# Kernel optimization log

Measured on AMD Instinct MI355X. Metric: run time of the kernel, lower is better.

## Reference

```python
import jax, jax.numpy as jnp
import numpy as np

N, C, H, K = 100000, 64, 8, 16
D = C // H  # head_dim = 8


def setup_inputs() -> dict:
    key = jax.random.key(0)
    ks = jax.random.split(key, 7)
    s = 1.0 / np.sqrt(C)
    return {
        "feats": jax.random.normal(ks[0], (N, C), jnp.float32),
        "knn_idx": jax.random.randint(ks[1], (N, K), 0, N, jnp.int32),
        "Wq": jax.random.normal(ks[2], (C, C), jnp.float32) * s,
        "Wk": jax.random.normal(ks[3], (C, C), jnp.float32) * s,
        "Wv": jax.random.normal(ks[4], (C, C), jnp.float32) * s,
        "Wo": jax.random.normal(ks[5], (C, C), jnp.float32) * s,
        "bo": jnp.zeros((C,), jnp.float32),
    }


def reference(feats, knn_idx, Wq, Wk, Wv, Wo, bo):
    # Projections (torch Linear y = x @ W^T expressed with pre-transposed W)
    q = (feats @ Wq).reshape(N, H, D)          # [N,H,D]
    k_feat = (feats @ Wk).reshape(N, H, D)     # [N,H,D]
    v = (feats @ Wv).reshape(N, H, D)          # [N,H,D]

    # Gather k-NN neighbors: [N,K,H,D]
    k_nb = k_feat[knn_idx]
    v_nb = v[knn_idx]

    # Scores: dot(q, k_neighbor) per head, scaled
    scores = jnp.einsum("nhd,nkhd->nkh", q, k_nb) / np.sqrt(D).astype(np.float32)
    attn = jax.nn.softmax(scores, axis=1)      # softmax over K neighbors

    out = jnp.einsum("nkh,nkhd->nhd", attn, v_nb).reshape(N, C)
    return out @ Wo + bo
```

## Files before the change

### kernel.cpp

```cpp
#include <hip/hip_runtime.h>
#include <hip/hip_fp16.h>
#include <math.h>

#define NPTS 100000
#define CDIM 64
#define KNN  16

typedef unsigned int uint;
typedef _Float16 f16x8 __attribute__((ext_vector_type(8)));
typedef float    f32x4 __attribute__((ext_vector_type(4)));

template <int CTRL>
__device__ __forceinline__ float dpp_add(float x) {
    int yi = __builtin_amdgcn_mov_dpp(__float_as_int(x), CTRL, 0xF, 0xF, true);
    return x + __int_as_float(yi);
}


__global__ __launch_bounds__(256) void pack_w(
    const float* __restrict__ Wq, const float* __restrict__ Wk,
    const float* __restrict__ Wv, const float* __restrict__ Wo,
    __half* __restrict__ frag)
{
    const float* Ws[4] = {Wq, Wk, Wv, Wo};
    f16x8* fp = (f16x8*)frag;
    const int e = blockIdx.x * 256 + threadIdx.x;
    const int lane = e & 63;
    const int ks   = (e >> 6) & 1;
    const int ct   = (e >> 7) & 3;
    const int mat  = e >> 9;
    const int m = lane & 15, quad = lane >> 4;
    const float* W = Ws[mat];
    f16x8 b;
    #pragma unroll
    for (int j = 0; j < 8; ++j)
        b[j] = (_Float16)W[(size_t)(ks * 32 + quad * 8 + j) * 64 + ct * 16 + m];
    fp[e] = b;
}

__device__ __forceinline__ f16x8 load_bfeat(const float* fp, int ks, int quad) {
    const float4 x0 = *(const float4*)(fp + ks * 32 + quad * 8);
    const float4 x1 = *(const float4*)(fp + ks * 32 + quad * 8 + 4);
    f16x8 a;
    a[0] = (_Float16)x0.x; a[1] = (_Float16)x0.y;
    a[2] = (_Float16)x0.z; a[3] = (_Float16)x0.w;
    a[4] = (_Float16)x1.x; a[5] = (_Float16)x1.y;
    a[6] = (_Float16)x1.z; a[7] = (_Float16)x1.w;
    return a;
}

__global__ __launch_bounds__(256) void proj_qkv(
    const float* __restrict__ feats, const __half* __restrict__ frag,
    __half* __restrict__ q, uint* __restrict__ kv)
{
    const int wid = blockIdx.x * 4 + (threadIdx.x >> 6);
    if (wid >= NPTS / 16) return;
    const int lane = threadIdx.x & 63;
    const int m = lane & 15, quad = lane >> 4;

    const f16x8* fp = (const f16x8*)frag;
    f16x8 Wf[3][4][2];
    #pragma unroll
    for (int mat = 0; mat < 3; ++mat)
        #pragma unroll
        for (int ct = 0; ct < 4; ++ct)
            #pragma unroll
            for (int ks = 0; ks < 2; ++ks)
                Wf[mat][ct][ks] = fp[((mat * 4 + ct) * 2 + ks) * 64 + lane];

    const int r0 = wid * 16;
    const float* ap = feats + (size_t)(r0 + m) * 64;
    const f16x8 Bf0 = load_bfeat(ap, 0, quad);
    const f16x8 Bf1 = load_bfeat(ap, 1, quad);

    const size_t pt = (size_t)(r0 + m);

    #pragma unroll
    for (int ct = 0; ct < 4; ++ct) {
        f32x4 aq = {0.f, 0.f, 0.f, 0.f};
        f32x4 ak = {0.f, 0.f, 0.f, 0.f};
        f32x4 av = {0.f, 0.f, 0.f, 0.f};
        aq = __builtin_amdgcn_mfma_f32_16x16x32_f16(Wf[0][ct][0], Bf0, aq, 0, 0, 0);
        aq = __builtin_amdgcn_mfma_f32_16x16x32_f16(Wf[0][ct][1], Bf1, aq, 0, 0, 0);
        ak = __builtin_amdgcn_mfma_f32_16x16x32_f16(Wf[1][ct][0], Bf0, ak, 0, 0, 0);
        ak = __builtin_amdgcn_mfma_f32_16x16x32_f16(Wf[1][ct][1], Bf1, ak, 0, 0, 0);
        av = __builtin_amdgcn_mfma_f32_16x16x32_f16(Wf[2][ct][0], Bf0, av, 0, 0, 0);
        av = __builtin_amdgcn_mfma_f32_16x16x32_f16(Wf[2][ct][1], Bf1, av, 0, 0, 0);

        const int ch = ct * 16 + quad * 4;
        uint2 qp;
        qp.x = (uint)__half_as_ushort(__float2half(aq[0]))
             | ((uint)__half_as_ushort(__float2half(aq[1])) << 16);
        qp.y = (uint)__half_as_ushort(__float2half(aq[2]))
             | ((uint)__half_as_ushort(__float2half(aq[3])) << 16);
        *(uint2*)(q + pt * 64 + ch) = qp;
        uint4 kp;
        kp.x = (uint)__half_as_ushort(__float2half(ak[0]))
             | ((uint)__half_as_ushort(__float2half(av[0])) << 16);
        kp.y = (uint)__half_as_ushort(__float2half(ak[1]))
             | ((uint)__half_as_ushort(__float2half(av[1])) << 16);
        kp.z = (uint)__half_as_ushort(__float2half(ak[2]))
             | ((uint)__half_as_ushort(__float2half(av[2])) << 16);
        kp.w = (uint)__half_as_ushort(__float2half(ak[3]))
             | ((uint)__half_as_ushort(__float2half(av[3])) << 16);
        *(uint4*)(kv + pt * 64 + ch) = kp;
    }
}

__global__ __launch_bounds__(256) void attn_out(
    const __half* __restrict__ q, const uint* __restrict__ kv,
    const int* __restrict__ knn, const __half* __restrict__ frag,
    const float* __restrict__ bo, float* __restrict__ out)
{
    __shared__ float sO[16][68];
    const int t = threadIdx.x;
    const int lane = t & 63;
    const int w = t >> 6;
    const int m = lane & 15, quad = lane >> 4;

    const f16x8* fpb = (const f16x8*)frag;
    const f16x8 Wf0 = fpb[((3 * 4 + w) * 2 + 0) * 64 + lane];
    const f16x8 Wf1 = fpb[((3 * 4 + w) * 2 + 1) * 64 + lane];

    const int n0 = blockIdx.x * 16;
    const float SC = 0.3535533905932738f * 1.4426950408889634f;

    #pragma unroll 1
    for (int p = 0; p < 4; ++p) {
        const int n = n0 + w * 4 + p;
        const int ns = __builtin_amdgcn_readfirstlane(n);

        const float qv = __half2float(q[(size_t)n * 64 + lane]);

        const int* kr = knn + (size_t)ns * KNN;
        int idx[KNN];
        #pragma unroll
        for (int i = 0; i < KNN; ++i) idx[i] = kr[i];

        uint u[KNN];
        #pragma unroll
        for (int i = 0; i < KNN; ++i) u[i] = kv[(size_t)idx[i] * 64 + lane];

        float sc[KNN], vr[KNN];
        #pragma unroll
        for (int i = 0; i < KNN; ++i) {
            const float2 kvf = __half22float2(*(const __half2*)&u[i]);
            vr[i] = kvf.y;
            float pr = qv * kvf.x;
            pr = dpp_add<0xB1>(pr);
            pr = dpp_add<0x4E>(pr);
            pr = dpp_add<0x141>(pr);
            sc[i] = __builtin_amdgcn_exp2f(pr * SC);
        }

        float s = 0.f;
        #pragma unroll
        for (int i = 0; i < KNN; ++i) s += sc[i];
        const float inv = 1.f / s;

        float acc = 0.f;
        #pragma unroll
        for (int i = 0; i < KNN; ++i) acc += sc[i] * vr[i];

        sO[w * 4 + p][lane] = acc * inv;
    }
    __syncthreads();

    f16x8 Bf0, Bf1;
    {
        const float* ap = &sO[m][0];
        const float4 x0 = *(const float4*)(ap + quad * 8);
        const float4 x1 = *(const float4*)(ap + quad * 8 + 4);
        Bf0[0] = (_Float16)x0.x; Bf0[1] = (_Float16)x0.y;
        Bf0[2] = (_Float16)x0.z; Bf0[3] = (_Float16)x0.w;
        Bf0[4] = (_Float16)x1.x; Bf0[5] = (_Float16)x1.y;
        Bf0[6] = (_Float16)x1.z; Bf0[7] = (_Float16)x1.w;
        const float4 y0 = *(const float4*)(ap + 32 + quad * 8);
        const float4 y1 = *(const float4*)(ap + 32 + quad * 8 + 4);
        Bf1[0] = (_Float16)y0.x; Bf1[1] = (_Float16)y0.y;
        Bf1[2] = (_Float16)y0.z; Bf1[3] = (_Float16)y0.w;
        Bf1[4] = (_Float16)y1.x; Bf1[5] = (_Float16)y1.y;
        Bf1[6] = (_Float16)y1.z; Bf1[7] = (_Float16)y1.w;
    }

    f32x4 ac = {0.f, 0.f, 0.f, 0.f};
    ac = __builtin_amdgcn_mfma_f32_16x16x32_f16(Wf0, Bf0, ac, 0, 0, 0);
    ac = __builtin_amdgcn_mfma_f32_16x16x32_f16(Wf1, Bf1, ac, 0, 0, 0);

    const int ch = w * 16 + quad * 4;
    const float4 bias = *(const float4*)(bo + ch);
    float4 o;
    o.x = ac[0] + bias.x; o.y = ac[1] + bias.y;
    o.z = ac[2] + bias.z; o.w = ac[3] + bias.w;
    *(float4*)(out + (size_t)(n0 + m) * 64 + ch) = o;
}

extern "C" void kernel_launch(void* const* d_in, const int* in_sizes, int n_in,
                              void* d_out, int out_size, void* d_ws, size_t ws_size,
                              hipStream_t stream) {
    const float* feats = (const float*)d_in[0];
    const int*   knn   = (const int*)d_in[1];
    const float* Wq    = (const float*)d_in[2];
    const float* Wk    = (const float*)d_in[3];
    const float* Wv    = (const float*)d_in[4];
    const float* Wo    = (const float*)d_in[5];
    const float* bo    = (const float*)d_in[6];
    float* out = (float*)d_out;

    __half* frag = (__half*)d_ws;
    __half* q_h  = (__half*)((char*)d_ws + 32768);
    uint*   kvb  = (uint*)((char*)d_ws + 32768 +
                           (size_t)NPTS * CDIM * sizeof(__half));

    pack_w<<<8, 256, 0, stream>>>(Wq, Wk, Wv, Wo, frag);
    proj_qkv<<<(NPTS / 16 + 3) / 4, 256, 0, stream>>>(feats, frag, q_h, kvb);
    attn_out<<<NPTS / 16, 256, 0, stream>>>(q_h, kvb, knn, frag, bo, out);
}
```

Baseline: 158.6 us.

## Process two points per wave with packed fp16 attention math and folded Q scale

The attention kernel now handles two points per wavefront, each half-wave covering one point with 2 channels per lane. Gathers become 8-byte loads, and dot products and the weighted V accumulation use packed half2 arithmetic with fewer DPP steps. The softmax scale is folded into the fp16 Wq fragments, and conversions use cvt_pkrtz. The projection kernel now processes two 16-row tiles per wave. Doing more of the math in fp16, with round-toward-zero conversion, lowers accuracy, and the output MFMA wastes half its rows.

```diff
diff --git a/kernel.cpp b/kernel.cpp
--- a/kernel.cpp
+++ b/kernel.cpp
@@ -11,9 +11,16 @@
 typedef float    f32x4 __attribute__((ext_vector_type(4)));
 
 template <int CTRL>
-__device__ __forceinline__ float dpp_add(float x) {
-    int yi = __builtin_amdgcn_mov_dpp(__float_as_int(x), CTRL, 0xF, 0xF, true);
-    return x + __int_as_float(yi);
+__device__ __forceinline__ __half dpp_add_h(__half x) {
+    int xi = (int)__half_as_ushort(x);
+    int yi = __builtin_amdgcn_mov_dpp(xi, CTRL, 0xF, 0xF, true);
+    return __hadd(x, __ushort_as_half((unsigned short)yi));
+}
+
+__device__ __forceinline__ uint pkrtz(float a, float b) {
+    union { __fp16 __attribute__((ext_vector_type(2))) h; uint u; } cv;
+    cv.h = __builtin_amdgcn_cvt_pkrtz(a, b);
+    return cv.u;
 }
 
 
@@ -23,6 +30,7 @@
     __half* __restrict__ frag)
 {
     const float* Ws[4] = {Wq, Wk, Wv, Wo};
+    const float scale[4] = {0.3535533905932738f * 1.4426950408889634f, 1.f, 1.f, 1.f};
     f16x8* fp = (f16x8*)frag;
     const int e = blockIdx.x * 256 + threadIdx.x;
     const int lane = e & 63;
@@ -31,10 +39,11 @@
     const int mat  = e >> 9;
     const int m = lane & 15, quad = lane >> 4;
     const float* W = Ws[mat];
+    const float sc = scale[mat];
     f16x8 b;
     #pragma unroll
     for (int j = 0; j < 8; ++j)
-        b[j] = (_Float16)W[(size_t)(ks * 32 + quad * 8 + j) * 64 + ct * 16 + m];
+        b[j] = (_Float16)(sc * W[(size_t)(ks * 32 + quad * 8 + j) * 64 + ct * 16 + m]);
     fp[e] = b;
 }
 
@@ -54,7 +63,6 @@
     __half* __restrict__ q, uint* __restrict__ kv)
 {
     const int wid = blockIdx.x * 4 + (threadIdx.x >> 6);
-    if (wid >= NPTS / 16) return;
     const int lane = threadIdx.x & 63;
     const int m = lane & 15, quad = lane >> 4;
 
@@ -68,42 +76,40 @@
             for (int ks = 0; ks < 2; ++ks)
                 Wf[mat][ct][ks] = fp[((mat * 4 + ct) * 2 + ks) * 64 + lane];
 
-    const int r0 = wid * 16;
-    const float* ap = feats + (size_t)(r0 + m) * 64;
-    const f16x8 Bf0 = load_bfeat(ap, 0, quad);
-    const f16x8 Bf1 = load_bfeat(ap, 1, quad);
-
-    const size_t pt = (size_t)(r0 + m);
-
-    #pragma unroll
-    for (int ct = 0; ct < 4; ++ct) {
-        f32x4 aq = {0.f, 0.f, 0.f, 0.f};
-        f32x4 ak = {0.f, 0.f, 0.f, 0.f};
-        f32x4 av = {0.f, 0.f, 0.f, 0.f};
-        aq = __builtin_amdgcn_mfma_f32_16x16x32_f16(Wf[0][ct][0], Bf0, aq, 0, 0, 0);
-        aq = __builtin_amdgcn_mfma_f32_16x16x32_f16(Wf[0][ct][1], Bf1, aq, 0, 0, 0);
-        ak = __builtin_amdgcn_mfma_f32_16x16x32_f16(Wf[1][ct][0], Bf0, ak, 0, 0, 0);
-        ak = __builtin_amdgcn_mfma_f32_16x16x32_f16(Wf[1][ct][1], Bf1, ak, 0, 0, 0);
-        av = __builtin_amdgcn_mfma_f32_16x16x32_f16(Wf[2][ct][0], Bf0, av, 0, 0, 0);
-        av = __builtin_amdgcn_mfma_f32_16x16x32_f16(Wf[2][ct][1], Bf1, av, 0, 0, 0);
-
-        const int ch = ct * 16 + quad * 4;
-        uint2 qp;
-        qp.x = (uint)__half_as_ushort(__float2half(aq[0]))
-             | ((uint)__half_as_ushort(__float2half(aq[1])) << 16);
-        qp.y = (uint)__half_as_ushort(__float2half(aq[2]))
-             | ((uint)__half_as_ushort(__float2half(aq[3])) << 16);
-        *(uint2*)(q + pt * 64 + ch) = qp;
-        uint4 kp;
-        kp.x = (uint)__half_as_ushort(__float2half(ak[0]))
-             | ((uint)__half_as_ushort(__float2half(av[0])) << 16);
-        kp.y = (uint)__half_as_ushort(__float2half(ak[1]))
-             | ((uint)__half_as_ushort(__float2half(av[1])) << 16);
-        kp.z = (uint)__half_as_ushort(__float2half(ak[2]))
-             | ((uint)__half_as_ushort(__float2half(av[2])) << 16);
-        kp.w = (uint)__half_as_ushort(__float2half(ak[3]))
-             | ((uint)__half_as_ushort(__float2half(av[3])) << 16);
-        *(uint4*)(kv + pt * 64 + ch) = kp;
+    #pragma unroll
+    for (int tt = 0; tt < 2; ++tt) {
+        const int tile = wid * 2 + tt;
+        if (tile >= NPTS / 16) break;
+        const int r0 = tile * 16;
+        const float* ap = feats + (size_t)(r0 + m) * 64;
+        const f16x8 Bf0 = load_bfeat(ap, 0, quad);
+        const f16x8 Bf1 = load_bfeat(ap, 1, quad);
+        const size_t pt = (size_t)(r0 + m);
+
+        #pragma unroll
+        for (int ct = 0; ct < 4; ++ct) {
+            f32x4 aq = {0.f, 0.f, 0.f, 0.f};
+            f32x4 ak = {0.f, 0.f, 0.f, 0.f};
+            f32x4 av = {0.f, 0.f, 0.f, 0.f};
+            aq = __builtin_amdgcn_mfma_f32_16x16x32_f16(Wf[0][ct][0], Bf0, aq, 0, 0, 0);
+            aq = __builtin_amdgcn_mfma_f32_16x16x32_f16(Wf[0][ct][1], Bf1, aq, 0, 0, 0);
+            ak = __builtin_amdgcn_mfma_f32_16x16x32_f16(Wf[1][ct][0], Bf0, ak, 0, 0, 0);
+            ak = __builtin_amdgcn_mfma_f32_16x16x32_f16(Wf[1][ct][1], Bf1, ak, 0, 0, 0);
+            av = __builtin_amdgcn_mfma_f32_16x16x32_f16(Wf[2][ct][0], Bf0, av, 0, 0, 0);
+            av = __builtin_amdgcn_mfma_f32_16x16x32_f16(Wf[2][ct][1], Bf1, av, 0, 0, 0);
+
+            const int ch = ct * 16 + quad * 4;
+            uint2 qp;
+            qp.x = pkrtz(aq[0], aq[1]);
+            qp.y = pkrtz(aq[2], aq[3]);
+            *(uint2*)(q + pt * 64 + ch) = qp;
+            uint4 kp;
+            kp.x = pkrtz(ak[0], av[0]);
+            kp.y = pkrtz(ak[1], av[1]);
+            kp.z = pkrtz(ak[2], av[2]);
+            kp.w = pkrtz(ak[3], av[3]);
+            *(uint4*)(kv + pt * 64 + ch) = kp;
+        }
     }
 }
 
@@ -112,87 +118,82 @@
     const int* __restrict__ knn, const __half* __restrict__ frag,
     const float* __restrict__ bo, float* __restrict__ out)
 {
-    __shared__ float sO[16][68];
+    __shared__ uint sO[8][36];
     const int t = threadIdx.x;
     const int lane = t & 63;
     const int w = t >> 6;
+    const int l32 = lane & 31;
+    const int p = lane >> 5;
     const int m = lane & 15, quad = lane >> 4;
 
     const f16x8* fpb = (const f16x8*)frag;
     const f16x8 Wf0 = fpb[((3 * 4 + w) * 2 + 0) * 64 + lane];
     const f16x8 Wf1 = fpb[((3 * 4 + w) * 2 + 1) * 64 + lane];
 
-    const int n0 = blockIdx.x * 16;
-    const float SC = 0.3535533905932738f * 1.4426950408889634f;
-
-    #pragma unroll 1
-    for (int p = 0; p < 4; ++p) {
-        const int n = n0 + w * 4 + p;
-        const int ns = __builtin_amdgcn_readfirstlane(n);
-
-        const float qv = __half2float(q[(size_t)n * 64 + lane]);
-
-        const int* kr = knn + (size_t)ns * KNN;
-        int idx[KNN];
-        #pragma unroll
-        for (int i = 0; i < KNN; ++i) idx[i] = kr[i];
-
-        uint u[KNN];
-        #pragma unroll
-        for (int i = 0; i < KNN; ++i) u[i] = kv[(size_t)idx[i] * 64 + lane];
-
-        float sc[KNN], vr[KNN];
-        #pragma unroll
-        for (int i = 0; i < KNN; ++i) {
-            const float2 kvf = __half22float2(*(const __half2*)&u[i]);
-            vr[i] = kvf.y;
-            float pr = qv * kvf.x;
-            pr = dpp_add<0xB1>(pr);
-            pr = dpp_add<0x4E>(pr);
-            pr = dpp_add<0x141>(pr);
-            sc[i] = __builtin_amdgcn_exp2f(pr * SC);
-        }
-
-        float s = 0.f;
-        #pragma unroll
-        for (int i = 0; i < KNN; ++i) s += sc[i];
-        const float inv = 1.f / s;
-
-        float acc = 0.f;
-        #pragma unroll
-        for (int i = 0; i < KNN; ++i) acc += sc[i] * vr[i];
-
-        sO[w * 4 + p][lane] = acc * inv;
+    const int n0 = blockIdx.x * 8;
+    const int nA = n0 + w * 2;
+    const int nB = nA + 1;
+    const int n  = nA + p;
+
+    const int* krA = knn + (size_t)nA * KNN;
+    const int* krB = knn + (size_t)nB * KNN;
+    int idx[KNN];
+    #pragma unroll
+    for (int i = 0; i < KNN; ++i) idx[i] = p ? krB[i] : krA[i];
+
+    const uint qw = ((const uint*)q)[(size_t)n * 32 + l32];
+    const __half2 qh = *(const __half2*)&qw;
+
+    uint2 u[KNN];
+    #pragma unroll
+    for (int i = 0; i < KNN; ++i)
+        u[i] = *(const uint2*)(kv + (size_t)idx[i] * 64 + 2 * l32);
+
+    float sc[KNN];
+    __half2 vh[KNN];
+    #pragma unroll
+    for (int i = 0; i < KNN; ++i) {
+        const uint kk = __builtin_amdgcn_perm(u[i].y, u[i].x, 0x05040100u);
+        const uint vv = __builtin_amdgcn_perm(u[i].y, u[i].x, 0x07060302u);
+        vh[i] = *(const __half2*)&vv;
+        const __half2 pr = __hmul2(qh, *(const __half2*)&kk);
+        __half s = __hadd(__low2half(pr), __high2half(pr));
+        s = dpp_add_h<0xB1>(s);
+        s = dpp_add_h<0x4E>(s);
+        sc[i] = __builtin_amdgcn_exp2f(__half2float(s));
     }
+
+    float ssum = 0.f;
+    #pragma unroll
+    for (int i = 0; i < KNN; ++i) ssum += sc[i];
+    const float inv = __builtin_amdgcn_rcpf(ssum);
+
+    __half2 acc = __float2half2_rn(0.f);
+    #pragma unroll
+    for (int i = 0; i < KNN; ++i)
+        acc = __hfma2(__float2half2_rn(sc[i]), vh[i], acc);
+    acc = __hmul2(acc, __float2half2_rn(inv));
+
+    sO[w * 2 + p][l32] = *(const uint*)&acc;
     __syncthreads();
 
-    f16x8 Bf0, Bf1;
-    {
-        const float* ap = &sO[m][0];
-        const float4 x0 = *(const float4*)(ap + quad * 8);
-        const float4 x1 = *(const float4*)(ap + quad * 8 + 4);
-        Bf0[0] = (_Float16)x0.x; Bf0[1] = (_Float16)x0.y;
-        Bf0[2] = (_Float16)x0.z; Bf0[3] = (_Float16)x0.w;
-        Bf0[4] = (_Float16)x1.x; Bf0[5] = (_Float16)x1.y;
-        Bf0[6] = (_Float16)x1.z; Bf0[7] = (_Float16)x1.w;
-        const float4 y0 = *(const float4*)(ap + 32 + quad * 8);
-        const float4 y1 = *(const float4*)(ap + 32 + quad * 8 + 4);
-        Bf1[0] = (_Float16)y0.x; Bf1[1] = (_Float16)y0.y;
-        Bf1[2] = (_Float16)y0.z; Bf1[3] = (_Float16)y0.w;
-        Bf1[4] = (_Float16)y1.x; Bf1[5] = (_Float16)y1.y;
-        Bf1[6] = (_Float16)y1.z; Bf1[7] = (_Float16)y1.w;
+    const uint4 ow = *(const uint4*)&sO[m & 7][quad * 4];
+    const f16x8 Bf = *(const f16x8*)&ow;
+
+    f32x4 ac = {0.f, 0.f, 0.f, 0.f};
+    ac = __builtin_amdgcn_mfma_f32_16x16x32_f16(Wf0, Bf, ac, 0, 0, 0);
+    const uint4 ow2 = *(const uint4*)&sO[m & 7][16 + quad * 4];
+    const f16x8 Bf2 = *(const f16x8*)&ow2;
+    ac = __builtin_amdgcn_mfma_f32_16x16x32_f16(Wf1, Bf2, ac, 0, 0, 0);
+
+    if (m < 8) {
+        const int ch = w * 16 + quad * 4;
+        const float4 bias = *(const float4*)(bo + ch);
+        float4 o;
+        o.x = ac[0] + bias.x; o.y = ac[1] + bias.y;
+        o.z = ac[2] + bias.z; o.w = ac[3] + bias.w;
+        *(float4*)(out + (size_t)(n0 + m) * 64 + ch) = o;
     }
-
-    f32x4 ac = {0.f, 0.f, 0.f, 0.f};
-    ac = __builtin_amdgcn_mfma_f32_16x16x32_f16(Wf0, Bf0, ac, 0, 0, 0);
-    ac = __builtin_amdgcn_mfma_f32_16x16x32_f16(Wf1, Bf1, ac, 0, 0, 0);
-
-    const int ch = w * 16 + quad * 4;
-    const float4 bias = *(const float4*)(bo + ch);
-    float4 o;
-    o.x = ac[0] + bias.x; o.y = ac[1] + bias.y;
-    o.z = ac[2] + bias.z; o.w = ac[3] + bias.w;
-    *(float4*)(out + (size_t)(n0 + m) * 64 + ch) = o;
 }
 
 extern "C" void kernel_launch(void* const* d_in, const int* in_sizes, int n_in,
@@ -213,6 +214,6 @@
                            (size_t)NPTS * CDIM * sizeof(__half));
 
     pack_w<<<8, 256, 0, stream>>>(Wq, Wk, Wv, Wo, frag);
-    proj_qkv<<<(NPTS / 16 + 3) / 4, 256, 0, stream>>>(feats, frag, q_h, kvb);
-    attn_out<<<NPTS / 16, 256, 0, stream>>>(q_h, kvb, knn, frag, bo, out);
-}
+    proj_qkv<<<782, 256, 0, stream>>>(feats, frag, q_h, kvb);
+    attn_out<<<NPTS / 8, 256, 0, stream>>>(q_h, kvb, knn, frag, bo, out);
+}
```

After: 153.6 us. -3.1%, faster.
